# Performance work log

Measured on AMD Instinct MI355X. Metric: run time of the kernel, lower is better.

Reference implementation:

```python
import jax, jax.numpy as jnp
import numpy as np

D = 1024      # n_embedding
H = 16        # n_head
DH = D // H   # head_size = 64
T = 2048      # block_size / seq len
B = 2
EPS = 1e-5


def layer_norm(x, gamma, beta):
    mu = jnp.mean(x, axis=-1, keepdims=True)
    var = jnp.mean((x - mu) ** 2, axis=-1, keepdims=True)
    return (x - mu) * jax.lax.rsqrt(var + EPS) * gamma + beta


def setup_inputs() -> dict:
    key = jax.random.key(0)
    ks = jax.random.split(key, 12)
    s = 0.02
    return {
        "x": jax.random.normal(ks[0], (B, T, D), jnp.float32),
        # per-head QKV projections stacked over heads: [H, D, DH] (no bias, as in Head)
        "wq": jax.random.normal(ks[1], (H, D, DH), jnp.float32) * s,
        "wk": jax.random.normal(ks[2], (H, D, DH), jnp.float32) * s,
        "wv": jax.random.normal(ks[3], (H, D, DH), jnp.float32) * s,
        # output projection [H*DH, D] with bias
        "w_proj": jax.random.normal(ks[4], (H * DH, D), jnp.float32) * s,
        "b_proj": jnp.zeros((D,), jnp.float32),
        # feedforward: D -> 4D -> D
        "w1": jax.random.normal(ks[5], (D, 4 * D), jnp.float32) * s,
        "b1": jnp.zeros((4 * D,), jnp.float32),
        "w2": jax.random.normal(ks[6], (4 * D, D), jnp.float32) * s,
        "b2": jnp.zeros((D,), jnp.float32),
        # layer norms
        "ln1_g": jnp.ones((D,), jnp.float32),
        "ln1_b": jnp.zeros((D,), jnp.float32),
        "ln2_g": jnp.ones((D,), jnp.float32),
        "ln2_b": jnp.zeros((D,), jnp.float32),
    }


def reference(x, wq, wk, wv, w_proj, b_proj, w1, b1, w2, b2,
              ln1_g, ln1_b, ln2_g, ln2_b):
    # pre-LN attention sub-block
    xn = layer_norm(x, ln1_g, ln1_b)                      # [B,T,D]
    q = jnp.einsum('btd,hdk->bhtk', xn, wq)               # [B,H,T,DH]
    k = jnp.einsum('btd,hdk->bhtk', xn, wk)
    v = jnp.einsum('btd,hdk->bhtk', xn, wv)
    scale = DH ** -0.5
    scores = jnp.einsum('bhtk,bhsk->bhts', q, k) * scale  # [B,H,T,T]
    causal = jnp.tril(jnp.ones((T, T), bool))
    scores = jnp.where(causal, scores, -jnp.inf)
    attn = jax.nn.softmax(scores, axis=-1)
    out = jnp.einsum('bhts,bhsk->bhtk', attn, v)          # [B,H,T,DH]
    out = out.transpose(0, 2, 1, 3).reshape(B, T, H * DH)  # concat heads
    x = x + out @ w_proj + b_proj                          # residual 1
    # pre-LN feedforward sub-block
    xn2 = layer_norm(x, ln2_g, ln2_b)
    h = jax.nn.relu(xn2 @ w1 + b1)
    x = x + h @ w2 + b2                                    # residual 2
    return x
```

## Files before the change

kernel.cpp:

```cpp
#include <hip/hip_runtime.h>
#include <hip/hip_bf16.h>
#include <math.h>


#define D_MODEL 1024
#define NH 16
#define DHEAD 64
#define SEQ 2048
#define NTOK 4096

typedef __bf16 bf16x8 __attribute__((ext_vector_type(8)));
typedef float f32x4 __attribute__((ext_vector_type(4)));
typedef unsigned short u16x8 __attribute__((ext_vector_type(8)));

__device__ __forceinline__ unsigned short f2b(float f) {
  unsigned u = __builtin_bit_cast(unsigned, f);
  u = u + 0x7fffu + ((u >> 16) & 1u);
  return (unsigned short)(u >> 16);
}

__device__ __forceinline__ bf16x8 ld_bf16x8(const unsigned short* p) {
  u16x8 u = *(const u16x8*)p;
  return __builtin_bit_cast(bf16x8, u);
}

__device__ __forceinline__ void async16(void* lds, const void* g) {
  __builtin_amdgcn_global_load_lds(
      (const __attribute__((address_space(1))) unsigned int*)g,
      (__attribute__((address_space(3))) unsigned int*)lds, 16, 0, 0);
}

__device__ __forceinline__ bf16x8 ds_read16(const void* p) {
  bf16x8 r;
  unsigned a = (unsigned)(size_t)(const __attribute__((address_space(3))) void*)p;
  asm volatile("ds_read_b128 %0, %1" : "=v"(r) : "v"(a));
  return r;
}
__device__ __forceinline__ void ds_write16b(void* p, unsigned short v) {
  unsigned a = (unsigned)(size_t)(__attribute__((address_space(3))) void*)p;
  unsigned vv = v;
  asm volatile("ds_write_b16 %0, %1" :: "v"(a), "v"(vv));
}
#define WAIT_LGKM0_FENCE() do { \
  asm volatile("s_waitcnt lgkmcnt(0)" ::: "memory"); \
  __builtin_amdgcn_sched_barrier(0); } while (0)


__global__ __launch_bounds__(256) void repack_qkv(
    const float* __restrict__ wq, const float* __restrict__ wk,
    const float* __restrict__ wv, unsigned short* __restrict__ outT) {
  __shared__ float tile[64][65];
  int t = blockIdx.x;
  int sel = t >> 8;
  int h = (t >> 4) & 15;
  int rt = t & 15;
  const float* in = (sel == 0 ? wq : sel == 1 ? wk : wv) + (size_t)h * D_MODEL * DHEAD;
  int d0 = rt * 64;
  for (int i = 0; i < 16; i++) {
    int idx = i * 256 + threadIdx.x;
    int r = idx >> 6, c = idx & 63;
    tile[r][c] = in[(size_t)(d0 + r) * DHEAD + c];
  }
  __syncthreads();
  unsigned short* ob = outT + (size_t)(sel * 1024 + h * 64) * D_MODEL + d0;
  for (int i = 0; i < 16; i++) {
    int idx = i * 256 + threadIdx.x;
    int c = idx >> 6, r = idx & 63;
    ob[(size_t)c * D_MODEL + r] = f2b(tile[r][c]);
  }
}

__global__ __launch_bounds__(256) void transpose_to_bf16(
    const float* __restrict__ in, unsigned short* __restrict__ out, int R, int C) {
  __shared__ float tile[64][65];
  int r0 = blockIdx.x * 64, c0 = blockIdx.y * 64;
  for (int i = 0; i < 16; i++) {
    int idx = i * 256 + threadIdx.x;
    int r = idx >> 6, c = idx & 63;
    tile[r][c] = in[(size_t)(r0 + r) * C + c0 + c];
  }
  __syncthreads();
  for (int i = 0; i < 16; i++) {
    int idx = i * 256 + threadIdx.x;
    int c = idx >> 6, r = idx & 63;
    out[(size_t)(c0 + c) * R + r0 + r] = f2b(tile[r][c]);
  }
}

__global__ __launch_bounds__(256) void layernorm_bf16(
    const float* __restrict__ x, const float* __restrict__ g,
    const float* __restrict__ bta, unsigned short* __restrict__ out) {
  int row = blockIdx.x;
  int tid = threadIdx.x;
  const float4* xr = (const float4*)(x + (size_t)row * D_MODEL);
  float4 v = xr[tid];
  float s = v.x + v.y + v.z + v.w;
  float s2 = v.x * v.x + v.y * v.y + v.z * v.z + v.w * v.w;
  for (int m = 1; m < 64; m <<= 1) {
    s += __shfl_xor(s, m);
    s2 += __shfl_xor(s2, m);
  }
  __shared__ float ps[4], ps2[4];
  int wid = tid >> 6;
  if ((tid & 63) == 0) { ps[wid] = s; ps2[wid] = s2; }
  __syncthreads();
  float S = ps[0] + ps[1] + ps[2] + ps[3];
  float S2 = ps2[0] + ps2[1] + ps2[2] + ps2[3];
  float mu = S * (1.f / D_MODEL);
  float var = S2 * (1.f / D_MODEL) - mu * mu;
  float inv = rsqrtf(var + 1e-5f);
  float4 gv = ((const float4*)g)[tid];
  float4 bv = ((const float4*)bta)[tid];
  ushort4 o;
  o.x = f2b((v.x - mu) * inv * gv.x + bv.x);
  o.y = f2b((v.y - mu) * inv * gv.y + bv.y);
  o.z = f2b((v.z - mu) * inv * gv.z + bv.z);
  o.w = f2b((v.w - mu) * inv * gv.w + bv.w);
  ((ushort4*)(out + (size_t)row * D_MODEL))[tid] = o;
}

template <int MODE>
__global__ __launch_bounds__(256, 2) void gemm_bt(
    const unsigned short* __restrict__ A, const unsigned short* __restrict__ BT,
    int M, int N, int K,
    const float* __restrict__ bias, const float* __restrict__ resid,
    float* __restrict__ outF, unsigned short* __restrict__ outB,
    unsigned short* __restrict__ outQ, unsigned short* __restrict__ outK,
    unsigned short* __restrict__ outV) {
  __shared__ alignas(16) unsigned short lsA[128 * 64];
  __shared__ alignas(16) unsigned short lsB[128 * 64];
  const int tid = threadIdx.x;
  const int wid = tid >> 6, lane = tid & 63;
  const int lr = lane & 15, lg = lane >> 4;
  const int row0 = blockIdx.x * 128, col0 = blockIdx.y * 128;
  const int wr = (wid >> 1) * 64, wc = (wid & 1) * 64;
  f32x4 acc[4][4] = {};
  const int nk = K >> 6;
  for (int kt = 0; kt < nk; ++kt) {
    const int k0 = kt << 6;
    if (kt) __syncthreads();
#pragma unroll
    for (int i = 0; i < 4; i++) {
      int sidx = i * 256 + tid;
      int r = sidx >> 3, s = sidx & 7;
      int ss = s ^ (r & 7);
      async16((char*)lsA + (i * 256 + wid * 64) * 16,
              A + (size_t)(row0 + r) * K + k0 + ss * 8);
      async16((char*)lsB + (i * 256 + wid * 64) * 16,
              BT + (size_t)(col0 + r) * K + k0 + ss * 8);
    }
    __syncthreads();
#pragma unroll
    for (int kk = 0; kk < 2; ++kk) {
      bf16x8 af[4], bfr[4];
#pragma unroll
      for (int m = 0; m < 4; m++) {
        int r = wr + m * 16 + lr;
        int sw = (kk * 4 + lg) ^ (r & 7);
        af[m] = *(const bf16x8*)((const char*)lsA + r * 128 + sw * 16);
      }
#pragma unroll
      for (int n = 0; n < 4; n++) {
        int r = wc + n * 16 + lr;
        int sw = (kk * 4 + lg) ^ (r & 7);
        bfr[n] = *(const bf16x8*)((const char*)lsB + r * 128 + sw * 16);
      }
#pragma unroll
      for (int m = 0; m < 4; m++)
#pragma unroll
        for (int n = 0; n < 4; n++)
          acc[m][n] = __builtin_amdgcn_mfma_f32_16x16x32_bf16(af[m], bfr[n], acc[m][n], 0, 0, 0);
    }
  }
#pragma unroll
  for (int m = 0; m < 4; m++) {
#pragma unroll
    for (int n = 0; n < 4; n++) {
#pragma unroll
      for (int r2 = 0; r2 < 4; r2++) {
        int row = row0 + wr + m * 16 + lg * 4 + r2;
        int col = col0 + wc + n * 16 + lr;
        float v = acc[m][n][r2];
        if constexpr (MODE == 0) {
          v += bias[col] + resid[(size_t)row * N + col];
          outF[(size_t)row * N + col] = v;
        } else if constexpr (MODE == 1) {
          v += bias[col];
          v = fmaxf(v, 0.f);
          outB[(size_t)row * N + col] = f2b(v);
        } else {
          int sel = col >> 10, jj = col & 1023, h = jj >> 6, dh = jj & 63;
          int b = row >> 11, t = row & 2047;
          size_t bh = (size_t)(b * NH + h);
          if (sel == 0)      outQ[(bh * SEQ + t) * DHEAD + dh] = f2b(v);
          else if (sel == 1) outK[(bh * SEQ + t) * DHEAD + dh] = f2b(v);
          else               outV[(bh * DHEAD + dh) * SEQ + t] = f2b(v);
        }
      }
    }
  }
}

template <int TAG>
__global__ __launch_bounds__(512, 1) void gemm_bt8(
    const unsigned short* __restrict__ A, const unsigned short* __restrict__ BT,
    int M, int N, int K,
    const float* __restrict__ bias, const float* __restrict__ resid,
    float* __restrict__ outF) {
  __shared__ alignas(16) unsigned short lsA[3][128 * 64];
  __shared__ alignas(16) unsigned short lsB[3][128 * 64];
  const int tid = threadIdx.x;
  const int wid = tid >> 6, lane = tid & 63;
  const int lr = lane & 15, lg = lane >> 4;
  const int row0 = blockIdx.x * 128, col0 = blockIdx.y * 128;
  const int wr = (wid >> 2) * 64, wc = (wid & 3) * 32;
  f32x4 acc[4][2] = {};
  const int nk = K >> 6;

  auto STAGE = [&](int bi, int kt) {
    const int k0 = kt << 6;
#pragma unroll
    for (int i = 0; i < 2; i++) {
      int sidx = i * 512 + tid;
      int r = sidx >> 3, s = sidx & 7;
      int ss = s ^ (r & 7);
      async16((char*)lsA[bi] + (i * 512 + wid * 64) * 16,
              A + (size_t)(row0 + r) * K + k0 + ss * 8);
      async16((char*)lsB[bi] + (i * 512 + wid * 64) * 16,
              BT + (size_t)(col0 + r) * K + k0 + ss * 8);
    }
  };

  STAGE(0, 0);
  if (nk > 1) STAGE(1, 1);
  for (int kt = 0; kt < nk; ++kt) {
    const int cur = kt % 3;
    if (kt + 2 < nk) {
      STAGE((kt + 2) % 3, kt + 2);
      asm volatile("s_waitcnt vmcnt(8)" ::: "memory");
    } else if (kt + 1 < nk) {
      asm volatile("s_waitcnt vmcnt(4)" ::: "memory");
    } else {
      asm volatile("s_waitcnt vmcnt(0)" ::: "memory");
    }
    __builtin_amdgcn_s_barrier();
    __builtin_amdgcn_sched_barrier(0);
#pragma unroll
    for (int kk = 0; kk < 2; ++kk) {
      bf16x8 af[4], bfr[2];
#pragma unroll
      for (int m = 0; m < 4; m++) {
        int r = wr + m * 16 + lr;
        int sw = (kk * 4 + lg) ^ (r & 7);
        af[m] = ds_read16((const char*)lsA[cur] + r * 128 + sw * 16);
      }
#pragma unroll
      for (int n = 0; n < 2; n++) {
        int r = wc + n * 16 + lr;
        int sw = (kk * 4 + lg) ^ (r & 7);
        bfr[n] = ds_read16((const char*)lsB[cur] + r * 128 + sw * 16);
      }
      WAIT_LGKM0_FENCE();
      __builtin_amdgcn_s_setprio(1);
#pragma unroll
      for (int m = 0; m < 4; m++)
#pragma unroll
        for (int n = 0; n < 2; n++)
          acc[m][n] = __builtin_amdgcn_mfma_f32_16x16x32_bf16(af[m], bfr[n], acc[m][n], 0, 0, 0);
      __builtin_amdgcn_s_setprio(0);
    }
    __builtin_amdgcn_sched_barrier(0);
    __builtin_amdgcn_s_barrier();
  }
#pragma unroll
  for (int m = 0; m < 4; m++) {
#pragma unroll
    for (int n = 0; n < 2; n++) {
#pragma unroll
      for (int r2 = 0; r2 < 4; r2++) {
        int row = row0 + wr + m * 16 + lg * 4 + r2;
        int col = col0 + wc + n * 16 + lr;
        float v = acc[m][n][r2] + bias[col] + resid[(size_t)row * N + col];
        outF[(size_t)row * N + col] = v;
      }
    }
  }
}

__global__ __launch_bounds__(512, 2) void gemm256_bt(
    const unsigned short* __restrict__ A, const unsigned short* __restrict__ BT,
    int M, int N, int K, int ntn,
    const float* __restrict__ bias, unsigned short* __restrict__ outB) {
  __shared__ alignas(16) unsigned short ls[2][2][2][256 * 32];
  const int tid = threadIdx.x;
  const int wid = tid >> 6, lane = tid & 63;
  const int lr = lane & 15, lg = lane >> 4;
  const int nwg = gridDim.x;
  const int wg = (blockIdx.x & 7) * (nwg >> 3) + (blockIdx.x >> 3);
  const int row0 = (wg / ntn) * 256, col0 = (wg % ntn) * 256;
  const int mbase = (wid >> 2) * 128;
  const int nbase = (wid & 3) * 64;

  f32x4 acc[8][4] = {};

  auto STAGE = [&](int buf, int kh, int ab, int kt) {
    const unsigned short* src = ab ? (BT + (size_t)col0 * K) : (A + (size_t)row0 * K);
    const int kbase = kt * 64 + kh * 32;
    unsigned short* dst0 = &ls[buf][kh][ab][0];
#pragma unroll
    for (int c = 0; c < 2; c++) {
      int s = c * 512 + tid;
      int row = s >> 2, c2 = s & 3;
      int ss = c2 ^ ((row >> 1) & 3);
      async16(dst0 + (size_t)(c * 512 + wid * 64) * 8,
              src + (size_t)row * K + kbase + ss * 8);
    }
  };
  auto LDA = [&](bf16x8* a, int buf, int kk, int mh) {
#pragma unroll
    for (int i = 0; i < 4; i++) {
      int mrow = mbase + (mh * 4 + i) * 16 + lr;
      int ch = lg ^ ((mrow >> 1) & 3);
      a[i] = ds_read16(&ls[buf][kk][0][mrow * 32 + ch * 8]);
    }
  };
  auto LDB = [&](bf16x8* b, int buf, int kk) {
#pragma unroll
    for (int i = 0; i < 4; i++) {
      int brow = nbase + i * 16 + lr;
      int ch = lg ^ ((brow >> 1) & 3);
      b[i] = ds_read16(&ls[buf][kk][1][brow * 32 + ch * 8]);
    }
  };

  const int nk = K >> 6;
  STAGE(0, 0, 0, 0); STAGE(0, 0, 1, 0); STAGE(0, 1, 0, 0); STAGE(0, 1, 1, 0);
  asm volatile("s_waitcnt vmcnt(4)" ::: "memory");
  __builtin_amdgcn_s_barrier();

  for (int t = 0; t < nk; ++t) {
    const int cur = t & 1, nxt = cur ^ 1;
    const bool haveNext = (t + 1 < nk);
    bf16x8 a[4], b[4];
    LDA(a, cur, 0, 0); LDB(b, cur, 0);
    if (haveNext) STAGE(nxt, 0, 0, t + 1);
    __builtin_amdgcn_s_barrier();
    WAIT_LGKM0_FENCE();
    __builtin_amdgcn_s_setprio(1);
#pragma unroll
    for (int i = 0; i < 4; i++)
#pragma unroll
      for (int j = 0; j < 4; j++)
        acc[i][j] = __builtin_amdgcn_mfma_f32_16x16x32_bf16(a[i], b[j], acc[i][j], 0, 0, 0);
    __builtin_amdgcn_s_setprio(0);
    __builtin_amdgcn_s_barrier();
    LDA(a, cur, 0, 1);
    if (haveNext) {
      STAGE(nxt, 0, 1, t + 1);
      asm volatile("s_waitcnt vmcnt(4)" ::: "memory");
    } else {
      asm volatile("s_waitcnt vmcnt(0)" ::: "memory");
    }
    __builtin_amdgcn_s_barrier();
    WAIT_LGKM0_FENCE();
    __builtin_amdgcn_s_setprio(1);
#pragma unroll
    for (int i = 0; i < 4; i++)
#pragma unroll
      for (int j = 0; j < 4; j++)
        acc[4 + i][j] = __builtin_amdgcn_mfma_f32_16x16x32_bf16(a[i], b[j], acc[4 + i][j], 0, 0, 0);
    __builtin_amdgcn_s_setprio(0);
    __builtin_amdgcn_s_barrier();
    LDA(a, cur, 1, 0); LDB(b, cur, 1);
    if (haveNext) STAGE(nxt, 1, 0, t + 1);
    __builtin_amdgcn_s_barrier();
    WAIT_LGKM0_FENCE();
    __builtin_amdgcn_s_setprio(1);
#pragma unroll
    for (int i = 0; i < 4; i++)
#pragma unroll
      for (int j = 0; j < 4; j++)
        acc[i][j] = __builtin_amdgcn_mfma_f32_16x16x32_bf16(a[i], b[j], acc[i][j], 0, 0, 0);
    __builtin_amdgcn_s_setprio(0);
    __builtin_amdgcn_s_barrier();
    LDA(a, cur, 1, 1);
    if (haveNext) {
      STAGE(nxt, 1, 1, t + 1);
      asm volatile("s_waitcnt vmcnt(4)" ::: "memory");
    }
    __builtin_amdgcn_s_barrier();
    WAIT_LGKM0_FENCE();
    __builtin_amdgcn_s_setprio(1);
#pragma unroll
    for (int i = 0; i < 4; i++)
#pragma unroll
      for (int j = 0; j < 4; j++)
        acc[4 + i][j] = __builtin_amdgcn_mfma_f32_16x16x32_bf16(a[i], b[j], acc[4 + i][j], 0, 0, 0);
    __builtin_amdgcn_s_setprio(0);
    __builtin_amdgcn_s_barrier();
  }
#pragma unroll
  for (int mi = 0; mi < 8; mi++) {
#pragma unroll
    for (int ni = 0; ni < 4; ni++) {
#pragma unroll
      for (int r2 = 0; r2 < 4; r2++) {
        int row = row0 + mbase + mi * 16 + lg * 4 + r2;
        int col = col0 + nbase + ni * 16 + lr;
        float v = acc[mi][ni][r2] + bias[col];
        outB[(size_t)row * N + col] = f2b(fmaxf(v, 0.f));
      }
    }
  }
}

__global__ __launch_bounds__(256) void attn_fwd(
    const unsigned short* __restrict__ Q, const unsigned short* __restrict__ K,
    const unsigned short* __restrict__ VT, unsigned short* __restrict__ O) {
  __shared__ alignas(16) unsigned short Kl[2][4096];
  __shared__ alignas(16) unsigned short Vl[2][4096];
  __shared__ alignas(16) unsigned short Plds[4][16][72];
  const int tid = threadIdx.x, wid = tid >> 6, lane = tid & 63;
  const int lr = lane & 15, lg = lane >> 4;
  const int sid = (int)(blockIdx.x & 7) * 128 + (int)(blockIdx.x >> 3);
  const int bh = sid >> 5, qt = 31 - (sid & 31);
  const unsigned short* Qb = Q + (size_t)bh * SEQ * DHEAD;
  const unsigned short* Kb = K + (size_t)bh * SEQ * DHEAD;
  const unsigned short* Vb = VT + (size_t)bh * DHEAD * SEQ;
  const int q0 = qt * 64 + wid * 16;
  bf16x8 qf[2];
#pragma unroll
  for (int kk = 0; kk < 2; kk++)
    qf[kk] = ld_bf16x8(Qb + (size_t)(q0 + lr) * DHEAD + kk * 32 + lg * 8);
  float psum[4] = {0.f, 0.f, 0.f, 0.f};
  f32x4 o[4] = {};
  const float cs = 0.18033688011112042f;
  const int ntiles = qt + 1;

  auto STAGE = [&](unsigned short* Kd, unsigned short* Vd, int s0) {
#pragma unroll
    for (int c = 0; c < 2; c++) {
      int s = c * 256 + tid;
      int row = s >> 3, sl = s & 7;
      int ss = sl ^ (row & 7);
      async16((char*)Kd + (c * 256 + wid * 64) * 16,
              Kb + (size_t)(s0 + row) * DHEAD + ss * 8);
      async16((char*)Vd + (c * 256 + wid * 64) * 16,
              Vb + (size_t)row * SEQ + s0 + ss * 8);
    }
  };

  STAGE(Kl[0], Vl[0], 0);
  for (int t = 0; t < ntiles; ++t) {
    if (t + 1 < ntiles) {
      STAGE(Kl[(t + 1) & 1], Vl[(t + 1) & 1], (t + 1) * 64);
      asm volatile("s_waitcnt vmcnt(4)" ::: "memory");
    } else {
      asm volatile("s_waitcnt vmcnt(0)" ::: "memory");
    }
    __builtin_amdgcn_s_barrier();
    __builtin_amdgcn_sched_barrier(0);
    const unsigned short* Kc = Kl[t & 1];
    const unsigned short* Vc = Vl[t & 1];
    const int s0 = t * 64;
    bf16x8 kfr[4][2], vfr[2][4];
#pragma unroll
    for (int n = 0; n < 4; n++)
#pragma unroll
      for (int kk = 0; kk < 2; kk++) {
        int r = n * 16 + lr;
        int ch = (kk * 4 + lg) ^ (r & 7);
        kfr[n][kk] = ds_read16((const char*)Kc + r * 128 + ch * 16);
      }
#pragma unroll
    for (int kk2 = 0; kk2 < 2; kk2++)
#pragma unroll
      for (int j = 0; j < 4; j++) {
        int r = j * 16 + lr;
        int ch = (kk2 * 4 + lg) ^ (r & 7);
        vfr[kk2][j] = ds_read16((const char*)Vc + r * 128 + ch * 16);
      }
    WAIT_LGKM0_FENCE();
    f32x4 sf[4];
#pragma unroll
    for (int n = 0; n < 4; n++) {
      f32x4 a = {};
      a = __builtin_amdgcn_mfma_f32_16x16x32_bf16(qf[0], kfr[n][0], a, 0, 0, 0);
      a = __builtin_amdgcn_mfma_f32_16x16x32_bf16(qf[1], kfr[n][1], a, 0, 0, 0);
      sf[n] = a;
    }
    const bool needMask = (s0 + 63 > q0);
    float p[4][4];
#pragma unroll
    for (int n = 0; n < 4; n++)
#pragma unroll
      for (int r = 0; r < 4; r++) {
        float x = sf[n][r] * cs;
        if (needMask && (s0 + n * 16 + lr > q0 + lg * 4 + r)) x = -INFINITY;
        float e = __builtin_amdgcn_exp2f(x);
        p[n][r] = e;
        psum[r] += e;
      }
#pragma unroll
    for (int n = 0; n < 4; n++)
#pragma unroll
      for (int r = 0; r < 4; r++)
        ds_write16b(&Plds[wid][lg * 4 + r][n * 16 + lr], f2b(p[n][r]));
    WAIT_LGKM0_FENCE();
    bf16x8 pa0 = ds_read16(&Plds[wid][lr][lg * 8]);
    bf16x8 pa1 = ds_read16(&Plds[wid][lr][32 + lg * 8]);
    WAIT_LGKM0_FENCE();
#pragma unroll
    for (int j = 0; j < 4; j++)
      o[j] = __builtin_amdgcn_mfma_f32_16x16x32_bf16(pa0, vfr[0][j], o[j], 0, 0, 0);
#pragma unroll
    for (int j = 0; j < 4; j++)
      o[j] = __builtin_amdgcn_mfma_f32_16x16x32_bf16(pa1, vfr[1][j], o[j], 0, 0, 0);
    __builtin_amdgcn_sched_barrier(0);
    __builtin_amdgcn_s_barrier();
  }
  unsigned short* Ob = O + ((size_t)(bh >> 4) * SEQ + q0) * D_MODEL + (bh & 15) * DHEAD;
#pragma unroll
  for (int r = 0; r < 4; r++) {
    float s = psum[r];
    s += __shfl_xor(s, 1);
    s += __shfl_xor(s, 2);
    s += __shfl_xor(s, 4);
    s += __shfl_xor(s, 8);
    float inv = 1.f / s;
#pragma unroll
    for (int j = 0; j < 4; j++)
      Ob[(size_t)(lg * 4 + r) * D_MODEL + j * 16 + lr] = f2b(o[j][r] * inv);
  }
}


extern "C" void kernel_launch(void* const* d_in, const int* in_sizes, int n_in,
                              void* d_out, int out_size, void* d_ws, size_t ws_size,
                              hipStream_t stream) {
  const float* x = (const float*)d_in[0];
  const float* wq = (const float*)d_in[1];
  const float* wk = (const float*)d_in[2];
  const float* wv = (const float*)d_in[3];
  const float* w_proj = (const float*)d_in[4];
  const float* b_proj = (const float*)d_in[5];
  const float* w1 = (const float*)d_in[6];
  const float* b1 = (const float*)d_in[7];
  const float* w2 = (const float*)d_in[8];
  const float* b2 = (const float*)d_in[9];
  const float* ln1g = (const float*)d_in[10];
  const float* ln1b = (const float*)d_in[11];
  const float* ln2g = (const float*)d_in[12];
  const float* ln2b = (const float*)d_in[13];

  char* ws = (char*)d_ws;
  const size_t MB = 1024ull * 1024ull;
  unsigned short* xn = (unsigned short*)(ws + 0);
  unsigned short* Qb = (unsigned short*)(ws + 8 * MB);
  unsigned short* Kb = (unsigned short*)(ws + 16 * MB);
  unsigned short* VTb = (unsigned short*)(ws + 24 * MB);
  unsigned short* aout = (unsigned short*)(ws + 32 * MB);
  unsigned short* hbuf = (unsigned short*)(ws + 40 * MB);
  unsigned short* WqkvT = (unsigned short*)(ws + 72 * MB);
  unsigned short* wprojT = (unsigned short*)(ws + 78 * MB);
  unsigned short* w1T = (unsigned short*)(ws + 80 * MB);
  unsigned short* w2T = (unsigned short*)(ws + 88 * MB);
  float* x1 = (float*)d_out;

  repack_qkv<<<dim3(768), 256, 0, stream>>>(wq, wk, wv, WqkvT);
  transpose_to_bf16<<<dim3(16, 16), 256, 0, stream>>>(w_proj, wprojT, 1024, 1024);
  transpose_to_bf16<<<dim3(16, 64), 256, 0, stream>>>(w1, w1T, 1024, 4096);
  transpose_to_bf16<<<dim3(64, 16), 256, 0, stream>>>(w2, w2T, 4096, 1024);

  layernorm_bf16<<<NTOK, 256, 0, stream>>>(x, ln1g, ln1b, xn);
  gemm_bt<2><<<dim3(32, 24), 256, 0, stream>>>(xn, WqkvT, NTOK, 3072, 1024,
      nullptr, nullptr, nullptr, nullptr, Qb, Kb, VTb);
  attn_fwd<<<dim3(1024), 256, 0, stream>>>(Qb, Kb, VTb, aout);
  gemm_bt8<0><<<dim3(32, 8), 512, 0, stream>>>(aout, wprojT, NTOK, 1024, 1024,
      b_proj, x, x1);
  layernorm_bf16<<<NTOK, 256, 0, stream>>>(x1, ln2g, ln2b, xn);
  gemm256_bt<<<dim3(256), 512, 0, stream>>>(xn, w1T, NTOK, 4096, 1024, 16,
      b1, hbuf);
  gemm_bt8<1><<<dim3(32, 8), 512, 0, stream>>>(hbuf, w2T, NTOK, 1024, 4096,
      b2, x1, (float*)d_out);
}
```

Before: 236.5 us.

## Restructure attention to 32x32 MFMA tiles with 128-row query blocks and register P

```diff
diff --git a/kernel.cpp b/kernel.cpp
--- a/kernel.cpp
+++ b/kernel.cpp
@@ -11,6 +11,7 @@
 
 typedef __bf16 bf16x8 __attribute__((ext_vector_type(8)));
 typedef float f32x4 __attribute__((ext_vector_type(4)));
+typedef float f32x16 __attribute__((ext_vector_type(16)));
 typedef unsigned short u16x8 __attribute__((ext_vector_type(8)));
 
 __device__ __forceinline__ unsigned short f2b(float f) {
@@ -36,10 +37,14 @@
   asm volatile("ds_read_b128 %0, %1" : "=v"(r) : "v"(a));
   return r;
 }
-__device__ __forceinline__ void ds_write16b(void* p, unsigned short v) {
+__device__ __forceinline__ void ds_write32(void* p, unsigned v) {
   unsigned a = (unsigned)(size_t)(__attribute__((address_space(3))) void*)p;
-  unsigned vv = v;
-  asm volatile("ds_write_b16 %0, %1" :: "v"(a), "v"(vv));
+  asm volatile("ds_write_b32 %0, %1" :: "v"(a), "v"(v));
+}
+__device__ __forceinline__ unsigned cvt_pk_bf16(float lo, float hi) {
+  unsigned d;
+  asm("v_cvt_pk_bf16_f32 %0, %1, %2" : "=v"(d) : "v"(lo), "v"(hi));
+  return d;
 }
 #define WAIT_LGKM0_FENCE() do { \
   asm volatile("s_waitcnt lgkmcnt(0)" ::: "memory"); \
@@ -414,28 +419,27 @@
   }
 }
 
-__global__ __launch_bounds__(256) void attn_fwd(
+__global__ __launch_bounds__(256, 4) void attn_fwd(
     const unsigned short* __restrict__ Q, const unsigned short* __restrict__ K,
     const unsigned short* __restrict__ VT, unsigned short* __restrict__ O) {
   __shared__ alignas(16) unsigned short Kl[2][4096];
   __shared__ alignas(16) unsigned short Vl[2][4096];
-  __shared__ alignas(16) unsigned short Plds[4][16][72];
   const int tid = threadIdx.x, wid = tid >> 6, lane = tid & 63;
-  const int lr = lane & 15, lg = lane >> 4;
-  const int sid = (int)(blockIdx.x & 7) * 128 + (int)(blockIdx.x >> 3);
-  const int bh = sid >> 5, qt = 31 - (sid & 31);
+  const int l31 = lane & 31, h = lane >> 5;
+  const int sid = (int)(blockIdx.x & 7) * 64 + (int)(blockIdx.x >> 3);
+  const int bh = sid >> 4, qt = 15 - (sid & 15);
   const unsigned short* Qb = Q + (size_t)bh * SEQ * DHEAD;
   const unsigned short* Kb = K + (size_t)bh * SEQ * DHEAD;
   const unsigned short* Vb = VT + (size_t)bh * DHEAD * SEQ;
-  const int q0 = qt * 64 + wid * 16;
-  bf16x8 qf[2];
-#pragma unroll
-  for (int kk = 0; kk < 2; kk++)
-    qf[kk] = ld_bf16x8(Qb + (size_t)(q0 + lr) * DHEAD + kk * 32 + lg * 8);
-  float psum[4] = {0.f, 0.f, 0.f, 0.f};
-  f32x4 o[4] = {};
+  const int q0w = qt * 128 + wid * 32;
+  bf16x8 qf[4];
+#pragma unroll
+  for (int dk = 0; dk < 4; dk++)
+    qf[dk] = ld_bf16x8(Qb + (size_t)(q0w + l31) * DHEAD + dk * 16 + h * 8);
+  f32x16 o0 = {}, o1 = {};
+  float psum = 0.f;
   const float cs = 0.18033688011112042f;
-  const int ntiles = qt + 1;
+  const int ntiles = qt * 2 + 2;
 
   auto STAGE = [&](unsigned short* Kd, unsigned short* Vd, int s0) {
 #pragma unroll
@@ -463,74 +467,102 @@
     const unsigned short* Kc = Kl[t & 1];
     const unsigned short* Vc = Vl[t & 1];
     const int s0 = t * 64;
-    bf16x8 kfr[4][2], vfr[2][4];
-#pragma unroll
-    for (int n = 0; n < 4; n++)
-#pragma unroll
-      for (int kk = 0; kk < 2; kk++) {
-        int r = n * 16 + lr;
-        int ch = (kk * 4 + lg) ^ (r & 7);
-        kfr[n][kk] = ds_read16((const char*)Kc + r * 128 + ch * 16);
-      }
-#pragma unroll
-    for (int kk2 = 0; kk2 < 2; kk2++)
-#pragma unroll
-      for (int j = 0; j < 4; j++) {
-        int r = j * 16 + lr;
-        int ch = (kk2 * 4 + lg) ^ (r & 7);
-        vfr[kk2][j] = ds_read16((const char*)Vc + r * 128 + ch * 16);
-      }
-    WAIT_LGKM0_FENCE();
-    f32x4 sf[4];
-#pragma unroll
-    for (int n = 0; n < 4; n++) {
-      f32x4 a = {};
-      a = __builtin_amdgcn_mfma_f32_16x16x32_bf16(qf[0], kfr[n][0], a, 0, 0, 0);
-      a = __builtin_amdgcn_mfma_f32_16x16x32_bf16(qf[1], kfr[n][1], a, 0, 0, 0);
-      sf[n] = a;
-    }
-    const bool needMask = (s0 + 63 > q0);
-    float p[4][4];
-#pragma unroll
-    for (int n = 0; n < 4; n++)
-#pragma unroll
-      for (int r = 0; r < 4; r++) {
-        float x = sf[n][r] * cs;
-        if (needMask && (s0 + n * 16 + lr > q0 + lg * 4 + r)) x = -INFINITY;
-        float e = __builtin_amdgcn_exp2f(x);
-        p[n][r] = e;
-        psum[r] += e;
-      }
-#pragma unroll
-    for (int n = 0; n < 4; n++)
-#pragma unroll
-      for (int r = 0; r < 4; r++)
-        ds_write16b(&Plds[wid][lg * 4 + r][n * 16 + lr], f2b(p[n][r]));
-    WAIT_LGKM0_FENCE();
-    bf16x8 pa0 = ds_read16(&Plds[wid][lr][lg * 8]);
-    bf16x8 pa1 = ds_read16(&Plds[wid][lr][32 + lg * 8]);
-    WAIT_LGKM0_FENCE();
-#pragma unroll
-    for (int j = 0; j < 4; j++)
-      o[j] = __builtin_amdgcn_mfma_f32_16x16x32_bf16(pa0, vfr[0][j], o[j], 0, 0, 0);
-#pragma unroll
-    for (int j = 0; j < 4; j++)
-      o[j] = __builtin_amdgcn_mfma_f32_16x16x32_bf16(pa1, vfr[1][j], o[j], 0, 0, 0);
+    if (s0 < q0w + 32) {
+      const bool needMask = (s0 + 63 > q0w);
+#pragma unroll
+      for (int g = 0; g < 2; g++) {
+        bf16x8 kf[4], vf[4];
+        {
+          int krow = 32 * g + l31;
+          int kbase_sw = krow & 7;
+#pragma unroll
+          for (int dk = 0; dk < 4; dk++) {
+            int ch = (2 * dk + h) ^ kbase_sw;
+            kf[dk] = ds_read16((const char*)Kc + krow * 128 + ch * 16);
+          }
+#pragma unroll
+          for (int dg = 0; dg < 2; dg++) {
+            int vrow = 32 * dg + l31;
+            int vsw = vrow & 7;
+#pragma unroll
+            for (int c = 0; c < 2; c++) {
+              int kk = 2 * g + c;
+              int ch = (2 * kk + h) ^ vsw;
+              vf[dg * 2 + c] = ds_read16((const char*)Vc + vrow * 128 + ch * 16);
+            }
+          }
+        }
+        WAIT_LGKM0_FENCE();
+        f32x16 st = {};
+#pragma unroll
+        for (int dk = 0; dk < 4; dk++)
+          st = __builtin_amdgcn_mfma_f32_32x32x16_bf16(kf[dk], qf[dk], st, 0, 0, 0);
+        float p[16];
+#pragma unroll
+        for (int reg = 0; reg < 16; reg++) {
+          float xx = st[reg] * cs;
+          if (needMask) {
+            int kg = s0 + 32 * g + (reg & 3) + 8 * (reg >> 2) + 4 * h;
+            if (kg > q0w + l31) xx = -INFINITY;
+          }
+          float e = __builtin_amdgcn_exp2f(xx);
+          p[reg] = e;
+          psum += e;
+        }
+        unsigned w[8];
+#pragma unroll
+        for (int s = 0; s < 4; s++) {
+          w[s * 2 + 0] = cvt_pk_bf16(p[s * 4 + 0], p[s * 4 + 1]);
+          w[s * 2 + 1] = cvt_pk_bf16(p[s * 4 + 2], p[s * 4 + 3]);
+        }
+#pragma unroll
+        for (int c = 0; c < 2; c++) {
+          unsigned a0 = w[(2 * c) * 2 + 0], b0 = w[(2 * c + 1) * 2 + 0];
+          unsigned a1 = w[(2 * c) * 2 + 1], b1 = w[(2 * c + 1) * 2 + 1];
+          asm volatile("v_permlane32_swap_b32 %0, %1" : "+v"(a0), "+v"(b0));
+          asm volatile("v_permlane32_swap_b32 %0, %1" : "+v"(a1), "+v"(b1));
+          uint4 pw = {a0, a1, b0, b1};
+          bf16x8 pf = __builtin_bit_cast(bf16x8, pw);
+          o0 = __builtin_amdgcn_mfma_f32_32x32x16_bf16(vf[0 * 2 + c], pf, o0, 0, 0, 0);
+          o1 = __builtin_amdgcn_mfma_f32_32x32x16_bf16(vf[1 * 2 + c], pf, o1, 0, 0, 0);
+        }
+      }
+    }
     __builtin_amdgcn_sched_barrier(0);
     __builtin_amdgcn_s_barrier();
   }
-  unsigned short* Ob = O + ((size_t)(bh >> 4) * SEQ + q0) * D_MODEL + (bh & 15) * DHEAD;
-#pragma unroll
-  for (int r = 0; r < 4; r++) {
-    float s = psum[r];
-    s += __shfl_xor(s, 1);
-    s += __shfl_xor(s, 2);
-    s += __shfl_xor(s, 4);
-    s += __shfl_xor(s, 8);
-    float inv = 1.f / s;
-#pragma unroll
-    for (int j = 0; j < 4; j++)
-      Ob[(size_t)(lg * 4 + r) * D_MODEL + j * 16 + lr] = f2b(o[j][r] * inv);
+  psum += __shfl_xor(psum, 32);
+  float inv = 1.f / psum;
+  unsigned short* slice = (unsigned short*)Kl + wid * 2048;
+#pragma unroll
+  for (int dg = 0; dg < 2; dg++) {
+#pragma unroll
+    for (int s = 0; s < 4; s++) {
+#pragma unroll
+      for (int m = 0; m < 2; m++) {
+        float va = (dg ? o1[s * 4 + 2 * m] : o0[s * 4 + 2 * m]) * inv;
+        float vb = (dg ? o1[s * 4 + 2 * m + 1] : o0[s * 4 + 2 * m + 1]) * inv;
+        unsigned wv = cvt_pk_bf16(va, vb);
+        int d = 32 * dg + 8 * s + 4 * h + 2 * m;
+        ds_write32(&slice[l31 * 64 + d], wv);
+      }
+    }
+  }
+  WAIT_LGKM0_FENCE();
+  bf16x8 ov[4];
+#pragma unroll
+  for (int pss = 0; pss < 4; pss++) {
+    int qrow = pss * 8 + (lane >> 3);
+    int d0 = (lane & 7) * 8;
+    ov[pss] = ds_read16(&slice[qrow * 64 + d0]);
+  }
+  WAIT_LGKM0_FENCE();
+  const int b = bh >> 4, head = bh & 15;
+#pragma unroll
+  for (int pss = 0; pss < 4; pss++) {
+    int qrow = pss * 8 + (lane >> 3);
+    int d0 = (lane & 7) * 8;
+    *(bf16x8*)(O + ((size_t)b * SEQ + q0w + qrow) * D_MODEL + head * DHEAD + d0) = ov[pss];
   }
 }
 
@@ -575,7 +607,7 @@
   layernorm_bf16<<<NTOK, 256, 0, stream>>>(x, ln1g, ln1b, xn);
   gemm_bt<2><<<dim3(32, 24), 256, 0, stream>>>(xn, WqkvT, NTOK, 3072, 1024,
       nullptr, nullptr, nullptr, nullptr, Qb, Kb, VTb);
-  attn_fwd<<<dim3(1024), 256, 0, stream>>>(Qb, Kb, VTb, aout);
+  attn_fwd<<<dim3(512), 256, 0, stream>>>(Qb, Kb, VTb, aout);
   gemm_bt8<0><<<dim3(32, 8), 512, 0, stream>>>(aout, wprojT, NTOK, 1024, 1024,
       b_proj, x, x1);
   layernorm_bf16<<<NTOK, 256, 0, stream>>>(x1, ln2g, ln2b, xn);
```

Result: no change. 232.3 us (-1.8%).
